# Optimization experiments

Hardware: AMD Instinct MI355X
Metric: run time of the kernel (lower is better)

## Reference

```python
import jax, jax.numpy as jnp
import numpy as np

B, H, W, C, HID, V, EMB = 16, 24, 96, 1024, 256, 5000, 256
BN_EPS = 1e-5


def _lin(k, fin, fout, s=0.05):
    return jax.random.normal(k, (fin, fout), jnp.float32) * s


def setup_inputs():
    ks = jax.random.split(jax.random.key(0), 24)
    inp = {
        "input_y": jax.random.randint(ks[0], (B,), 0, V),
        "input_hidden": jax.random.normal(ks[1], (B, 1, HID), jnp.float32),
        "img_feature": jax.random.normal(ks[2], (B, C, H, W), jnp.float32),
        "feature_w": W,
        "attention_sum": jnp.zeros((B, 1, H, W), jnp.float32),
        "alpha_t": jax.random.uniform(ks[3], (B, 1, H, W), jnp.float32),
        "feature_h": H,
        "batch_size": B,
        "h_mask": jax.random.randint(ks[4], (B,), 1, H + 1),
        "w_mask": jax.random.randint(ks[5], (B,), 1, W + 1),
        "emb_table": jax.random.normal(ks[6], (V, EMB), jnp.float32) * 0.05,
        "gru1_wi": _lin(ks[7], EMB, 3 * HID), "gru1_wh": _lin(ks[8], HID, 3 * HID),
        "gru1_bi": jnp.zeros((3 * HID,), jnp.float32), "gru1_bh": jnp.zeros((3 * HID,), jnp.float32),
        "fc1_w": _lin(ks[9], HID, 256), "fc1_b": jnp.zeros((256,), jnp.float32),
        "gru2_wi": _lin(ks[10], C, 3 * HID), "gru2_wh": _lin(ks[11], HID, 3 * HID),
        "gru2_bi": jnp.zeros((3 * HID,), jnp.float32), "gru2_bh": jnp.zeros((3 * HID,), jnp.float32),
        "out_w": _lin(ks[12], 128, V), "out_b": jnp.zeros((V,), jnp.float32),
        "emb2_w": _lin(ks[13], 256, 128), "emb2_b": jnp.zeros((128,), jnp.float32),
        "conv1_w": jax.random.normal(ks[14], (1, 1, 3, 3), jnp.float32) * 0.05,
        "conv1_b": jnp.zeros((1,), jnp.float32),
        "conv_tan_w": jax.random.normal(ks[15], (256, 256, 3, 3), jnp.float32) * 0.02,
        "conv_tan_b": jnp.zeros((256,), jnp.float32),
        "fc2_w": _lin(ks[16], HID, 128), "fc2_b": jnp.zeros((128,), jnp.float32),
        "ua_w": _lin(ks[17], C, 256), "ua_b": jnp.zeros((256,), jnp.float32),
        "uf_w": _lin(ks[18], 1, 256), "uf_b": jnp.zeros((256,), jnp.float32),
        "v_w": _lin(ks[19], 256, 1), "v_b": jnp.zeros((1,), jnp.float32),
        "wc_w": _lin(ks[20], C, 128), "wc_b": jnp.zeros((128,), jnp.float32),
        "bn1_gamma": jnp.ones((256,), jnp.float32), "bn1_beta": jnp.zeros((256,), jnp.float32),
        "bn1_mean": jnp.zeros((256,), jnp.float32), "bn1_var": jnp.ones((256,), jnp.float32),
    }
    return inp


def _gru(x, h, wi, wh, bi, bh):
    # PyTorch GRUCell semantics
    gi = x @ wi + bi
    gh = h @ wh + bh
    ir, iz, inn = jnp.split(gi, 3, axis=-1)
    hr, hz, hn = jnp.split(gh, 3, axis=-1)
    r = jax.nn.sigmoid(ir + hr)
    z = jax.nn.sigmoid(iz + hz)
    n = jnp.tanh(inn + r * hn)
    return (1.0 - z) * n + z * h


def _conv(x, w, b):
    y = jax.lax.conv_general_dilated(x, w, (1, 1), 'SAME',
                                     dimension_numbers=('NCHW', 'OIHW', 'NCHW'))
    return y + b[None, :, None, None]


def reference(input_y, input_hidden, img_feature, feature_w, attention_sum, alpha_t,
              feature_h, batch_size, h_mask, w_mask,
              emb_table, gru1_wi, gru1_wh, gru1_bi, gru1_bh, fc1_w, fc1_b,
              gru2_wi, gru2_wh, gru2_bi, gru2_bh, out_w, out_b, emb2_w, emb2_b,
              conv1_w, conv1_b, conv_tan_w, conv_tan_b, fc2_w, fc2_b,
              ua_w, ua_b, uf_w, uf_b, v_w, v_b, wc_w, wc_b,
              bn1_gamma, bn1_beta, bn1_mean, bn1_var):
    b, c, h, w = img_feature.shape
    # per-sample validity mask over the feature map  [B, H, W]
    et_mask = ((jnp.arange(h)[None, :] < h_mask[:, None])[:, :, None]
               & (jnp.arange(w)[None, :] < w_mask[:, None])[:, None, :]).astype(jnp.float32)

    emb = emb_table[input_y]                      # [B, 256] (dropout = identity, eval)
    h0 = input_hidden[:, 0, :]                    # [B, HID]
    st1 = _gru(emb, h0, gru1_wi, gru1_wh, gru1_bi, gru1_bh)
    st1 = st1 @ fc1_w + fc1_b                     # [B, 256]

    alpha_c = _conv(alpha_t, conv1_w, conv1_b)    # [B, 1, H, W]
    att_sum = attention_sum + alpha_c             # coverage accumulator

    img1 = jnp.einsum('bchw,cd->bhwd', img_feature, ua_w) + ua_b  # [B,H,W,256]
    att1 = att_sum[:, 0, :, :, None] * uf_w[0] + uf_b             # Linear(1,256)
    et = st1[:, None, None, :] + img1 + att1      # [B, H, W, 256]

    et_nchw = jnp.transpose(et, (0, 3, 1, 2))
    et_nchw = _conv(et_nchw, conv_tan_w, conv_tan_b)
    et_nchw = et_nchw * et_mask[:, None]
    inv = bn1_gamma / jnp.sqrt(bn1_var + BN_EPS)  # eval-mode BatchNorm2d(256)
    et_nchw = (et_nchw - bn1_mean[None, :, None, None]) * inv[None, :, None, None] \
              + bn1_beta[None, :, None, None]
    et_nchw = jnp.tanh(et_nchw)

    e = jnp.einsum('bchw,c->bhw', et_nchw, v_w[:, 0]) + v_b[0]    # [B, H, W]
    e_exp = jnp.exp(e) * et_mask
    e_sum = jnp.sum(e_exp, axis=(1, 2))
    alpha = e_exp / (e_sum[:, None, None] + 1e-8)                 # masked softmax

    ct = jnp.einsum('bhw,bchw->bc', alpha, img_feature)           # [B, 1024]
    st = _gru(ct, st1, gru2_wi, gru2_wh, gru2_bi, gru2_bh)        # [B, HID]
    hidden_next = st[:, None, :]

    pre = (st @ fc2_w + fc2_b) + (emb @ emb2_w + emb2_b) + (ct @ wc_w + wc_b)  # [B,128]
    output = jax.nn.log_softmax(pre @ out_w + out_b, axis=1)[:, None, :]       # [B,1,V]
    return output, hidden_next, alpha[:, None], att_sum
```

## Files before the change

kernel.cpp:

```cpp
#include <hip/hip_runtime.h>
#include <hip/hip_bf16.h>

#define B   16
#define H   24
#define W   96
#define C   1024
#define HID 256
#define V   5000
#define EMB 256
#define HW  (H*W)
#define BN_EPS 1e-5f
#define H2  (H+2)
#define W2  (W+2)

#define OUT0 0
#define OUT1 (B*V)
#define OUT2 (OUT1 + B*HID)
#define OUT3 (OUT2 + B*HW)

#define WSB_IMGT  0
#define WSB_ETP   75497472
#define WSB_WTB   96370688
#define WSB_UAT   97550336
#define WSB_E     98074624
#define WSB_ST1   98369536
#define WSB_CT    98385920
#define WSB_PRE   98451456
#define WSB_GIGH1 98459648
#define WSB_GH2   98574336
#define WSB_GI2   98631680

typedef __attribute__((ext_vector_type(8))) short short8;
typedef __attribute__((ext_vector_type(4))) float f32x4;

__device__ inline unsigned short f2bf(float f) {
    union { float f; unsigned int u; } v; v.f = f;
    unsigned int r = v.u + 0x7fffu + ((v.u >> 16) & 1u);
    return (unsigned short)(r >> 16);
}
__device__ inline float bf2f(unsigned short u) {
    union { unsigned int u; float f; } v; v.u = ((unsigned int)u) << 16;
    return v.f;
}

__global__ __launch_bounds__(256) void k_imgT(const float* img, unsigned short* imgT)
{
    int hw0 = blockIdx.x*64, c0 = blockIdx.y*128, b = blockIdx.z;
    int t = threadIdx.x;
    __shared__ __align__(16) unsigned short tr[64*256];
    int row = t & 63;
    int sgb = t >> 6;
    const float* src = img + ((size_t)b*C + c0)*HW + hw0 + row;
    #pragma unroll
    for (int k = 0; k < 4; ++k) {
        int sg = sgb + k*4;
        union { short8 v; unsigned short u[8]; } pk;
        #pragma unroll
        for (int j = 0; j < 8; ++j)
            pk.u[j] = f2bf(src[(size_t)(sg*8 + j)*HW]);
        *(short8*)&tr[row*256 + (sg ^ (row & 31))*8] = pk.v;
    }
    __syncthreads();
    #pragma unroll
    for (int k = 0; k < 4; ++k) {
        int i = k*256 + t;
        int orow = i >> 4, sg = i & 15;
        *(short8*)&imgT[((size_t)(b*HW) + hw0 + orow)*1024 + c0 + sg*8] =
            *(const short8*)&tr[orow*256 + (sg ^ (orow & 31))*8];
    }
}

__global__ __launch_bounds__(256) void k_prep(
    const float* conv_w_src, unsigned short* wtb,
    const float* ua_w, unsigned short* uat,
    const float* att_in, const float* alpha_t, const float* cw, const float* cb, float* att_out,
    float* ct, unsigned short* et_p)
{
    int x = blockIdx.x, t = threadIdx.x;
    if (x < 2304) {
        int idx = x*256 + t;
        int c = idx & 255; int o = (idx >> 8) & 255; int khw = idx >> 16;
        wtb[(khw*256 + o)*256 + c] = f2bf(conv_w_src[(o*256 + c)*9 + khw]);
    } else if (x < 3328) {
        int idx = (x - 2304)*256 + t;
        int c = idx & 1023; int d = idx >> 10;
        uat[d*1024 + c] = f2bf(ua_w[c*256 + d]);
    } else if (x < 3472) {
        int i = (x - 3328)*256 + t;
        int w = i % W; int h = (i / W) % H; int b = i / HW;
        float s = cb[0];
        #pragma unroll
        for (int kh = 0; kh < 3; ++kh) {
            int r = h + kh - 1; if (r < 0 || r >= H) continue;
            #pragma unroll
            for (int kw = 0; kw < 3; ++kw) {
                int c = w + kw - 1; if (c < 0 || c >= W) continue;
                s += alpha_t[(b*H + r)*W + c]*cw[kh*3+kw];
            }
        }
        att_out[i] = att_in[i] + s;
    } else if (x < 3536) {
        ct[(x - 3472)*256 + t] = 0.f;
    } else {
        int flat = (x - 3536)*256 + t;
        int b = flat / 7808; int r = flat - b*7808;
        int h2, w2, j;
        if (r < 3136)      { h2 = 0;  w2 = r >> 5;          j = r & 31; }
        else if (r < 6272) { h2 = 25; w2 = (r - 3136) >> 5; j = (r - 3136) & 31; }
        else {
            int rr = r - 6272;
            h2 = 1 + (rr >> 6);
            int s = rr & 63;
            w2 = (s < 32) ? 0 : 97;
            j = s & 31;
        }
        ((int4*)et_p)[((size_t)(b*H2 + h2)*W2 + w2)*32 + j] = make_int4(0,0,0,0);
    }
}

__global__ __launch_bounds__(256) void k_tail1(
    const int* y, const float* emb_table, const float* h0,
    const float* wi, const float* wh, float* gigh)
{
    int virt = blockIdx.x*16;
    int t = threadIdx.x;
    bool gi_mode = virt < 768;
    __shared__ float a_l[16*256];
    for (int i = t; i < 4096; i += 256) {
        int b = i >> 8, k = i & 255;
        a_l[i] = gi_mode ? emb_table[y[b]*EMB + k] : h0[b*HID + k];
    }
    __syncthreads();
    int nl = t & 15, b = t >> 4;
    int n = (gi_mode ? virt : virt - 768) + nl;
    const float* wp = gi_mode ? wi : wh;
    float acc = 0.f;
    #pragma unroll 16
    for (int k = 0; k < 256; ++k) acc += a_l[b*256 + k]*wp[k*768 + n];
    gigh[b*1536 + virt + nl] = acc;
}

__global__ __launch_bounds__(256) void k_fc1c(
    const float* gigh, const float* h0, const float* bi, const float* bh,
    const float* fc1_w, const float* fc1_b, float* st1)
{
    int n0 = blockIdx.x*16, t = threadIdx.x;
    __shared__ float a_l[16*256];
    for (int i = t; i < 4096; i += 256) {
        int b = i >> 8, k = i & 255;
        const float* g = gigh + b*1536;
        float ir = g[k] + bi[k], iz = g[256+k] + bi[256+k], in_ = g[512+k] + bi[512+k];
        float hr = g[768+k] + bh[k], hz = g[1024+k] + bh[256+k], hn = g[1280+k] + bh[512+k];
        float r = 1.f/(1.f+__expf(-(ir+hr)));
        float z = 1.f/(1.f+__expf(-(iz+hz)));
        float n = tanhf(in_ + r*hn);
        a_l[i] = (1.f - z)*n + z*h0[b*HID + k];
    }
    __syncthreads();
    int nl = t & 15, b = t >> 4;
    float acc = fc1_b[n0+nl];
    #pragma unroll 16
    for (int k = 0; k < 256; ++k) acc += a_l[b*256+k]*fc1_w[k*256 + n0 + nl];
    st1[b*256 + n0 + nl] = acc;
}

__global__ __launch_bounds__(256, 3) void k_et(
    const unsigned short* imgT, const unsigned short* uat, const float* ua_b,
    const float* st1, const float* att_sum, const float* uf_w, const float* uf_b,
    unsigned short* et_p)
{
    int h = blockIdx.x, ny = blockIdx.y, b = blockIdx.z;
    int t = threadIdx.x;
    int wv = t >> 6, lane = t & 63, q = lane >> 4, ln = lane & 15;
    int n0 = ny*128 + wv*32;
    __shared__ __align__(16) unsigned short a_l[96*256];

    f32x4 acc[12];
    #pragma unroll
    for (int i = 0; i < 12; ++i) acc[i] = (f32x4){0.f,0.f,0.f,0.f};

    const unsigned short* ab = imgT + ((size_t)(b*HW) + h*W)*1024;
    const unsigned short* bbase = uat + (size_t)(n0 + ln)*1024 + q*8;

    int sw8 = (q ^ ((ln & 7) << 2)) << 3;
    int ebase[6];
    #pragma unroll
    for (int mf = 0; mf < 6; ++mf) ebase[mf] = (ln + 16*mf)*256 + sw8;

    for (int c0 = 0; c0 < 1024; c0 += 128) {
        __syncthreads();
        #pragma unroll
        for (int i = t; i < 1536; i += 256) {
            int m = i >> 4, sg = i & 15;
            ((int4*)a_l)[m*32 + (sg ^ ((m & 7) << 2))] =
                *((const int4*)(ab + (size_t)m*1024 + c0) + sg);
        }
        __syncthreads();
        #pragma unroll
        for (int cs = 0; cs < 128; cs += 32) {
            short8 av[6];
            #pragma unroll
            for (int mf = 0; mf < 6; ++mf)
                av[mf] = *(const short8*)&a_l[ebase[mf] ^ cs];
            #pragma unroll
            for (int j = 0; j < 2; ++j) {
                short8 bv = *(const short8*)(bbase + (size_t)(j*16)*1024 + c0 + cs);
                #pragma unroll
                for (int mf = 0; mf < 6; ++mf)
                    acc[mf*2+j] = __builtin_amdgcn_mfma_f32_16x16x32_bf16(av[mf], bv, acc[mf*2+j], 0, 0, 0);
            }
        }
    }

    float att_m[24];
    #pragma unroll
    for (int mf = 0; mf < 6; ++mf)
        #pragma unroll
        for (int r = 0; r < 4; ++r)
            att_m[mf*4+r] = att_sum[(b*H + h)*W + mf*16 + q*4 + r];
    #pragma unroll
    for (int j = 0; j < 2; ++j) {
        int n = n0 + j*16 + ln;
        float s1 = st1[b*256 + n] + ua_b[n];
        float ufw = uf_w[n], ufb = uf_b[n];
        #pragma unroll
        for (int mf = 0; mf < 6; ++mf)
            #pragma unroll
            for (int r = 0; r < 4; ++r) {
                int m = mf*16 + q*4 + r;
                float v = acc[mf*2+j][r] + s1 + att_m[mf*4+r]*ufw + ufb;
                et_p[((size_t)(b*H2 + h + 1)*W2 + (m + 1))*256 + n] = f2bf(v);
            }
    }
}

__global__ __launch_bounds__(256, 3) void k_conv(
    const unsigned short* et_p, const unsigned short* wtb, const float* cb,
    const float* bn_g, const float* bn_b, const float* bn_m, const float* bn_v,
    const float* v_w, float* e_part)
{
    int h = blockIdx.x, ny = blockIdx.y, b = blockIdx.z;
    int t = threadIdx.x;
    int wv = t >> 6, lane = t & 63, q = lane >> 4, ln = lane & 15;
    int n0 = ny*128 + wv*32;
    __shared__ __align__(16) unsigned short patch[3*6400];
    __shared__ float lds_red[4][96];

    f32x4 acc[12];
    #pragma unroll
    for (int i = 0; i < 12; ++i) acc[i] = (f32x4){0.f,0.f,0.f,0.f};

    int abase[6][3];
    #pragma unroll
    for (int mf = 0; mf < 6; ++mf)
        #pragma unroll
        for (int kw = 0; kw < 3; ++kw) {
            int x2 = ln + 16*mf + kw;
            int sp0 = ((x2 & 3) << 3) | (q ^ (((x2 >> 2) & 3) << 1));
            abase[mf][kw] = (x2 >> 2)*256 + sp0*8;
        }

    for (int c0 = 0; c0 < 256; c0 += 64) {
        __syncthreads();
        for (int i = t; i < 2352; i += 256) {
            int kh = i / 784; int r = i - kh*784; int x2 = r >> 3; int sg = r & 7;
            const int4* src = (const int4*)et_p + ((size_t)(b*H2 + h + kh)*W2 + x2)*32 + (c0 >> 3) + sg;
            int sp = ((x2 & 3) << 3) | (sg ^ (((x2 >> 2) & 3) << 1));
            ((int4*)patch)[kh*800 + (x2 >> 2)*32 + sp] = *src;
        }
        __syncthreads();
        #pragma unroll
        for (int kh = 0; kh < 3; ++kh) {
            #pragma unroll
            for (int kw = 0; kw < 3; ++kw) {
                const unsigned short* brow = wtb + ((size_t)((kh*3 + kw)*256 + n0 + ln))*256 + c0 + q*8;
                #pragma unroll
                for (int cs = 0; cs < 64; cs += 32) {
                    short8 av[6];
                    #pragma unroll
                    for (int mf = 0; mf < 6; ++mf)
                        av[mf] = *(const short8*)&patch[kh*6400 + (abase[mf][kw] ^ cs)];
                    #pragma unroll
                    for (int j = 0; j < 2; ++j) {
                        short8 bv = *(const short8*)(brow + j*4096 + cs);
                        #pragma unroll
                        for (int mf = 0; mf < 6; ++mf)
                            acc[mf*2+j] = __builtin_amdgcn_mfma_f32_16x16x32_bf16(av[mf], bv, acc[mf*2+j], 0, 0, 0);
                    }
                }
            }
        }
    }

    float psum[24];
    #pragma unroll
    for (int i = 0; i < 24; ++i) psum[i] = 0.f;
    #pragma unroll
    for (int j = 0; j < 2; ++j) {
        int o = n0 + j*16 + ln;
        float inv  = bn_g[o]*rsqrtf(bn_v[o] + BN_EPS);
        float mean = bn_m[o], beta = bn_b[o], bias = cb[o], vw = v_w[o];
        #pragma unroll
        for (int mf = 0; mf < 6; ++mf)
            #pragma unroll
            for (int r = 0; r < 4; ++r) {
                float x = (acc[mf*2+j][r] + bias - mean)*inv + beta;
                x = fminf(fmaxf(x, -15.f), 15.f);
                float ex = __expf(2.f*x);
                psum[mf*4+r] += ((ex - 1.f)/(ex + 1.f))*vw;
            }
    }
    #pragma unroll
    for (int s = 1; s < 16; s <<= 1)
        #pragma unroll
        for (int i = 0; i < 24; ++i) psum[i] += __shfl_xor(psum[i], s);
    if (ln == 0) {
        #pragma unroll
        for (int mf = 0; mf < 6; ++mf)
            #pragma unroll
            for (int r = 0; r < 4; ++r)
                lds_red[wv][mf*16 + q*4 + r] = psum[mf*4+r];
    }
    __syncthreads();
    if (t < 96)
        e_part[(size_t)ny*(B*HW) + (b*H + h)*W + t] =
            lds_red[0][t] + lds_red[1][t] + lds_red[2][t] + lds_red[3][t];
}

__global__ __launch_bounds__(256) void k_softmax(
    const float* e_part, const int* h_mask, const int* w_mask, const float* v_b,
    float* alpha_out)
{
    int b = blockIdx.x, t = threadIdx.x;
    int hm = h_mask[b], wm = w_mask[b];
    float vb = v_b[0];
    __shared__ float red[256];
    float vals[9];
    float loc = 0.f;
    #pragma unroll
    for (int i = 0; i < 9; ++i) {
        int hw = t + i*256;
        int hh = hw / W, ww = hw % W;
        float v = 0.f;
        if (hh < hm && ww < wm)
            v = __expf(e_part[b*HW + hw] + e_part[B*HW + b*HW + hw] + vb);
        vals[i] = v; loc += v;
    }
    red[t] = loc; __syncthreads();
    for (int s = 128; s > 0; s >>= 1) { if (t < s) red[t] += red[t+s]; __syncthreads(); }
    float inv = 1.f/(red[0] + 1e-8f);
    #pragma unroll
    for (int i = 0; i < 9; ++i) alpha_out[b*HW + t + i*256] = vals[i]*inv;
}

__global__ __launch_bounds__(256) void k_ct(
    const float* alpha, const unsigned short* imgT, float* ct)
{
    int s = blockIdx.x, b = blockIdx.y, t = threadIdx.x;
    int cg = (t & 127)*8, half = t >> 7;
    float acc[8];
    #pragma unroll
    for (int j = 0; j < 8; ++j) acc[j] = 0.f;
    for (int i = 0; i < 72; ++i) {
        int hw = s*144 + i*2 + half;
        float a = alpha[b*HW + hw];
        union { short8 v; unsigned short u[8]; } pk;
        pk.v = *(const short8*)&imgT[((size_t)(b*HW) + hw)*1024 + cg];
        #pragma unroll
        for (int j = 0; j < 8; ++j) acc[j] += a*bf2f(pk.u[j]);
    }
    #pragma unroll
    for (int j = 0; j < 8; ++j) atomicAdd(&ct[b*1024 + cg + j], acc[j]);
}

__global__ __launch_bounds__(256) void k_g2(
    const float* st1, const int* y, const float* emb_table,
    const float* wh, const float* emb2_w, float* gh2,
    const float* ct, const float* wi, const float* wc_w, float* gi2p)
{
    int x = blockIdx.x, t = threadIdx.x;
    __shared__ float a_l[16*256];
    if (x < 56) {
        int virt = x*16;
        bool ghm = virt < 768;
        for (int i = t; i < 4096; i += 256) {
            int b = i >> 8, k = i & 255;
            a_l[i] = ghm ? st1[b*256 + k] : emb_table[y[b]*EMB + k];
        }
        __syncthreads();
        int nl = t & 15, b = t >> 4;
        float acc = 0.f;
        if (ghm) {
            int n = virt + nl;
            #pragma unroll 16
            for (int k = 0; k < 256; ++k) acc += a_l[b*256+k]*wh[k*768 + n];
        } else {
            int n = virt - 768 + nl;
            #pragma unroll 16
            for (int k = 0; k < 256; ++k) acc += a_l[b*256+k]*emb2_w[k*128 + n];
        }
        gh2[b*896 + virt + nl] = acc;
    } else {
        int xx = x - 56;
        int ks = xx / 56, virt = (xx - ks*56)*16;
        int k0 = ks*256;
        for (int i = t; i < 4096; i += 256) {
            int b = i >> 8, k = i & 255;
            a_l[i] = ct[b*1024 + k0 + k];
        }
        __syncthreads();
        int nl = t & 15, b = t >> 4;
        float acc = 0.f;
        if (virt < 768) {
            int n = virt + nl;
            #pragma unroll 16
            for (int k = 0; k < 256; ++k) acc += a_l[b*256+k]*wi[(k0+k)*768 + n];
        } else {
            int n = virt - 768 + nl;
            #pragma unroll 16
            for (int k = 0; k < 256; ++k) acc += a_l[b*256+k]*wc_w[(k0+k)*128 + n];
        }
        gi2p[(ks*16 + b)*896 + virt + nl] = acc;
    }
}

__global__ __launch_bounds__(256) void k_fc2c(
    const float* gi2p, const float* gh2, const float* st1,
    const float* bi, const float* bh,
    const float* fc2_w, const float* fc2_b, const float* emb2_b, const float* wc_b,
    float* hidden_out, float* pre)
{
    int n0 = blockIdx.x*16, t = threadIdx.x;
    __shared__ float st_l[16*256];
    for (int i = t; i < 4096; i += 256) {
        int b = i >> 8, k = i & 255;
        float ir = bi[k], iz = bi[256+k], in_ = bi[512+k];
        #pragma unroll
        for (int ks = 0; ks < 4; ++ks) {
            const float* g = gi2p + (ks*16 + b)*896;
            ir += g[k]; iz += g[256+k]; in_ += g[512+k];
        }
        const float* gh = gh2 + b*896;
        float hr = gh[k] + bh[k], hz = gh[256+k] + bh[256+k], hn = gh[512+k] + bh[512+k];
        float h = st1[b*256+k];
        float r = 1.f/(1.f+__expf(-(ir+hr)));
        float z = 1.f/(1.f+__expf(-(iz+hz)));
        float n = tanhf(in_ + r*hn);
        float s = (1.f - z)*n + z*h;
        st_l[i] = s;
        if (blockIdx.x == 0) hidden_out[b*HID + k] = s;
    }
    __syncthreads();
    int nl = t & 15, b = t >> 4;
    int n = n0 + nl;
    float acc = fc2_b[n] + emb2_b[n] + wc_b[n] + gh2[b*896 + 768 + n];
    #pragma unroll
    for (int ks = 0; ks < 4; ++ks) acc += gi2p[(ks*16 + b)*896 + 768 + n];
    #pragma unroll 16
    for (int k = 0; k < 256; ++k) acc += st_l[b*256+k]*fc2_w[k*128 + n];
    pre[b*128 + n] = acc;
}

__global__ __launch_bounds__(256) void k_logits(
    const float* pre, const float* out_w, const float* out_b, float* out)
{
    int j0 = blockIdx.x*64, t = threadIdx.x;
    __shared__ float pre_l[16*128];
    for (int i = t; i < 2048; i += 256) pre_l[i] = pre[i];
    __syncthreads();
    int jl = t & 63, bg = t >> 6;
    int j = j0 + jl;
    if (j >= V) return;
    float acc0=0.f, acc1=0.f, acc2=0.f, acc3=0.f;
    const float* pl = pre_l + bg*4*128;
    #pragma unroll 8
    for (int k = 0; k < 128; ++k) {
        float wv = out_w[k*V + j];
        acc0 += pl[k]*wv; acc1 += pl[128+k]*wv; acc2 += pl[256+k]*wv; acc3 += pl[384+k]*wv;
    }
    float ob = out_b[j];
    out[(bg*4+0)*V + j] = acc0 + ob;
    out[(bg*4+1)*V + j] = acc1 + ob;
    out[(bg*4+2)*V + j] = acc2 + ob;
    out[(bg*4+3)*V + j] = acc3 + ob;
}

__global__ __launch_bounds__(1024) void k_lsm(float* out)
{
    int b = blockIdx.x, t = threadIdx.x;
    __shared__ float red[1024];
    float lg[5]; float mx = -1e30f;
    #pragma unroll
    for (int i = 0; i < 5; ++i) {
        int j = t + i*1024;
        lg[i] = (j < V) ? out[b*V + j] : -1e30f;
        mx = fmaxf(mx, lg[i]);
    }
    red[t] = mx; __syncthreads();
    for (int s = 512; s > 0; s >>= 1) { if (t < s) red[t] = fmaxf(red[t], red[t+s]); __syncthreads(); }
    float gmax = red[0]; __syncthreads();
    float se = 0.f;
    #pragma unroll
    for (int i = 0; i < 5; ++i) { int j = t + i*1024; if (j < V) se += __expf(lg[i] - gmax); }
    red[t] = se; __syncthreads();
    for (int s = 512; s > 0; s >>= 1) { if (t < s) red[t] += red[t+s]; __syncthreads(); }
    float lse = logf(red[0]);
    #pragma unroll
    for (int i = 0; i < 5; ++i) { int j = t + i*1024; if (j < V) out[b*V + j] = lg[i] - gmax - lse; }
}

extern "C" void kernel_launch(void* const* d_in, const int* in_sizes, int n_in,
                              void* d_out, int out_size, void* d_ws, size_t ws_size,
                              hipStream_t stream)
{
    const int*   input_y      = (const int*)  d_in[0];
    const float* input_hidden = (const float*)d_in[1];
    const float* img          = (const float*)d_in[2];
    const float* attention    = (const float*)d_in[4];
    const float* alpha_t      = (const float*)d_in[5];
    const int*   h_mask       = (const int*)  d_in[8];
    const int*   w_mask       = (const int*)  d_in[9];
    const float* emb_table    = (const float*)d_in[10];
    const float* gru1_wi      = (const float*)d_in[11];
    const float* gru1_wh      = (const float*)d_in[12];
    const float* gru1_bi      = (const float*)d_in[13];
    const float* gru1_bh      = (const float*)d_in[14];
    const float* fc1_w        = (const float*)d_in[15];
    const float* fc1_b        = (const float*)d_in[16];
    const float* gru2_wi      = (const float*)d_in[17];
    const float* gru2_wh      = (const float*)d_in[18];
    const float* gru2_bi      = (const float*)d_in[19];
    const float* gru2_bh      = (const float*)d_in[20];
    const float* out_w        = (const float*)d_in[21];
    const float* out_b        = (const float*)d_in[22];
    const float* emb2_w       = (const float*)d_in[23];
    const float* emb2_b       = (const float*)d_in[24];
    const float* conv1_w      = (const float*)d_in[25];
    const float* conv1_b      = (const float*)d_in[26];
    const float* conv_tan_w   = (const float*)d_in[27];
    const float* conv_tan_b   = (const float*)d_in[28];
    const float* fc2_w        = (const float*)d_in[29];
    const float* fc2_b        = (const float*)d_in[30];
    const float* ua_w         = (const float*)d_in[31];
    const float* ua_b         = (const float*)d_in[32];
    const float* uf_w         = (const float*)d_in[33];
    const float* uf_b         = (const float*)d_in[34];
    const float* v_w          = (const float*)d_in[35];
    const float* v_b          = (const float*)d_in[36];
    const float* wc_w         = (const float*)d_in[37];
    const float* wc_b         = (const float*)d_in[38];
    const float* bn1_gamma    = (const float*)d_in[39];
    const float* bn1_beta     = (const float*)d_in[40];
    const float* bn1_mean     = (const float*)d_in[41];
    const float* bn1_var      = (const float*)d_in[42];

    float* out = (float*)d_out;
    char*  ws  = (char*)d_ws;
    unsigned short* imgT = (unsigned short*)(ws + WSB_IMGT);
    unsigned short* et_p = (unsigned short*)(ws + WSB_ETP);
    unsigned short* wtb  = (unsigned short*)(ws + WSB_WTB);
    unsigned short* uat  = (unsigned short*)(ws + WSB_UAT);
    float* e_part = (float*)(ws + WSB_E);
    float* st1   = (float*)(ws + WSB_ST1);
    float* ct    = (float*)(ws + WSB_CT);
    float* pre   = (float*)(ws + WSB_PRE);
    float* gigh1 = (float*)(ws + WSB_GIGH1);
    float* gh2   = (float*)(ws + WSB_GH2);
    float* gi2p  = (float*)(ws + WSB_GI2);

    float* out_logits = out + OUT0;
    float* out_hidden = out + OUT1;
    float* out_alpha  = out + OUT2;
    float* out_attsum = out + OUT3;

    k_imgT<<<dim3(HW/64, C/128, B), 256, 0, stream>>>(img, imgT);
    k_prep<<<4024, 256, 0, stream>>>(conv_tan_w, wtb, ua_w, uat,
                                     attention, alpha_t, conv1_w, conv1_b, out_attsum,
                                     ct, et_p);
    k_tail1<<<96, 256, 0, stream>>>(input_y, emb_table, input_hidden,
                                    gru1_wi, gru1_wh, gigh1);
    k_fc1c<<<16, 256, 0, stream>>>(gigh1, input_hidden, gru1_bi, gru1_bh,
                                   fc1_w, fc1_b, st1);
    k_et<<<dim3(H, 2, B), 256, 0, stream>>>(imgT, uat, ua_b, st1, out_attsum,
                                            uf_w, uf_b, et_p);
    k_conv<<<dim3(H, 2, B), 256, 0, stream>>>(et_p, wtb, conv_tan_b,
                                              bn1_gamma, bn1_beta, bn1_mean, bn1_var,
                                              v_w, e_part);
    k_softmax<<<B, 256, 0, stream>>>(e_part, h_mask, w_mask, v_b, out_alpha);
    k_ct<<<dim3(16, B), 256, 0, stream>>>(out_alpha, imgT, ct);
    k_g2<<<280, 256, 0, stream>>>(st1, input_y, emb_table, gru2_wh, emb2_w, gh2,
                                  ct, gru2_wi, wc_w, gi2p);
    k_fc2c<<<8, 256, 0, stream>>>(gi2p, gh2, st1, gru2_bi, gru2_bh,
                                  fc2_w, fc2_b, emb2_b, wc_b, out_hidden, pre);
    k_logits<<<(V + 63)/64, 256, 0, stream>>>(pre, out_w, out_b, out_logits);
    k_lsm<<<B, 1024, 0, stream>>>(out_logits);
}
```

Before: 546.9 us.

## Retile et/conv GEMMs to 2x2 wave grid and register-prefetch next LDS tile

Both the et projection and conv kernels change their per-wave tiling from 96 rows x 32 columns to a 2x2 wave grid of 48 rows x 64 columns each. This loads fewer A fragments from LDS per MFMA and reuses each global B fragment across fewer rows. The next K-chunk of the A tile is now prefetched into registers while the MFMAs of the current chunk run, so global load latency overlaps compute. The LDS swizzle patterns are also changed. The cost is higher register pressure from the prefetch buffers (10 int4 in conv), which may lower occupancy under launch_bounds(256,3).

```diff
diff --git a/kernel.cpp b/kernel.cpp
--- a/kernel.cpp
+++ b/kernel.cpp
@@ -172,7 +172,8 @@
     int h = blockIdx.x, ny = blockIdx.y, b = blockIdx.z;
     int t = threadIdx.x;
     int wv = t >> 6, lane = t & 63, q = lane >> 4, ln = lane & 15;
-    int n0 = ny*128 + wv*32;
+    int wm = wv & 1, wn = wv >> 1;
+    int n0 = ny*128 + wn*64;
     __shared__ __align__(16) unsigned short a_l[96*256];
 
     f32x4 acc[12];
@@ -182,53 +183,70 @@
     const unsigned short* ab = imgT + ((size_t)(b*HW) + h*W)*1024;
     const unsigned short* bbase = uat + (size_t)(n0 + ln)*1024 + q*8;
 
-    int sw8 = (q ^ ((ln & 7) << 2)) << 3;
-    int ebase[6];
-    #pragma unroll
-    for (int mf = 0; mf < 6; ++mf) ebase[mf] = (ln + 16*mf)*256 + sw8;
+    int slot0 = q ^ (ln & 7);
+    int ebase[3];
+    #pragma unroll
+    for (int mf = 0; mf < 3; ++mf)
+        ebase[mf] = (wm*48 + ln + 16*mf)*256 + slot0*8;
+
+    int4 pr[6];
+    #pragma unroll
+    for (int k = 0; k < 6; ++k) {
+        int i = t + k*256;
+        int m = i >> 4, sg = i & 15;
+        pr[k] = *((const int4*)(ab + (size_t)m*1024) + sg);
+    }
 
     for (int c0 = 0; c0 < 1024; c0 += 128) {
         __syncthreads();
         #pragma unroll
-        for (int i = t; i < 1536; i += 256) {
+        for (int k = 0; k < 6; ++k) {
+            int i = t + k*256;
             int m = i >> 4, sg = i & 15;
-            ((int4*)a_l)[m*32 + (sg ^ ((m & 7) << 2))] =
-                *((const int4*)(ab + (size_t)m*1024 + c0) + sg);
+            ((int4*)a_l)[m*32 + ((sg & 8) | ((sg ^ m) & 7))] = pr[k];
         }
         __syncthreads();
+        if (c0 < 896) {
+            #pragma unroll
+            for (int k = 0; k < 6; ++k) {
+                int i = t + k*256;
+                int m = i >> 4, sg = i & 15;
+                pr[k] = *((const int4*)(ab + (size_t)m*1024 + c0 + 128) + sg);
+            }
+        }
         #pragma unroll
         for (int cs = 0; cs < 128; cs += 32) {
-            short8 av[6];
-            #pragma unroll
-            for (int mf = 0; mf < 6; ++mf)
+            short8 av[3];
+            #pragma unroll
+            for (int mf = 0; mf < 3; ++mf)
                 av[mf] = *(const short8*)&a_l[ebase[mf] ^ cs];
             #pragma unroll
-            for (int j = 0; j < 2; ++j) {
+            for (int j = 0; j < 4; ++j) {
                 short8 bv = *(const short8*)(bbase + (size_t)(j*16)*1024 + c0 + cs);
                 #pragma unroll
-                for (int mf = 0; mf < 6; ++mf)
-                    acc[mf*2+j] = __builtin_amdgcn_mfma_f32_16x16x32_bf16(av[mf], bv, acc[mf*2+j], 0, 0, 0);
-            }
-        }
-    }
-
-    float att_m[24];
-    #pragma unroll
-    for (int mf = 0; mf < 6; ++mf)
+                for (int mf = 0; mf < 3; ++mf)
+                    acc[mf*4+j] = __builtin_amdgcn_mfma_f32_16x16x32_bf16(av[mf], bv, acc[mf*4+j], 0, 0, 0);
+            }
+        }
+    }
+
+    float att_m[12];
+    #pragma unroll
+    for (int mf = 0; mf < 3; ++mf)
         #pragma unroll
         for (int r = 0; r < 4; ++r)
-            att_m[mf*4+r] = att_sum[(b*H + h)*W + mf*16 + q*4 + r];
-    #pragma unroll
-    for (int j = 0; j < 2; ++j) {
+            att_m[mf*4+r] = att_sum[(b*H + h)*W + wm*48 + mf*16 + q*4 + r];
+    #pragma unroll
+    for (int j = 0; j < 4; ++j) {
         int n = n0 + j*16 + ln;
         float s1 = st1[b*256 + n] + ua_b[n];
         float ufw = uf_w[n], ufb = uf_b[n];
         #pragma unroll
-        for (int mf = 0; mf < 6; ++mf)
+        for (int mf = 0; mf < 3; ++mf)
             #pragma unroll
             for (int r = 0; r < 4; ++r) {
-                int m = mf*16 + q*4 + r;
-                float v = acc[mf*2+j][r] + s1 + att_m[mf*4+r]*ufw + ufb;
+                int m = wm*48 + mf*16 + q*4 + r;
+                float v = acc[mf*4+j][r] + s1 + att_m[mf*4+r]*ufw + ufb;
                 et_p[((size_t)(b*H2 + h + 1)*W2 + (m + 1))*256 + n] = f2bf(v);
             }
     }
@@ -242,33 +260,59 @@
     int h = blockIdx.x, ny = blockIdx.y, b = blockIdx.z;
     int t = threadIdx.x;
     int wv = t >> 6, lane = t & 63, q = lane >> 4, ln = lane & 15;
-    int n0 = ny*128 + wv*32;
+    int wm = wv & 1, wn = wv >> 1;
+    int n0 = ny*128 + wn*64;
     __shared__ __align__(16) unsigned short patch[3*6400];
-    __shared__ float lds_red[4][96];
+    __shared__ float lds_red[2][96];
 
     f32x4 acc[12];
     #pragma unroll
     for (int i = 0; i < 12; ++i) acc[i] = (f32x4){0.f,0.f,0.f,0.f};
 
-    int abase[6][3];
-    #pragma unroll
-    for (int mf = 0; mf < 6; ++mf)
+    int abase[3][3];
+    #pragma unroll
+    for (int mf = 0; mf < 3; ++mf)
         #pragma unroll
         for (int kw = 0; kw < 3; ++kw) {
-            int x2 = ln + 16*mf + kw;
-            int sp0 = ((x2 & 3) << 3) | (q ^ (((x2 >> 2) & 3) << 1));
+            int x2 = wm*48 + ln + 16*mf + kw;
+            int sp0 = ((x2 & 3) << 3) | ((q ^ (x2 & 7)) & 7);
             abase[mf][kw] = (x2 >> 2)*256 + sp0*8;
         }
+
+    const int4* ebase_g = (const int4*)et_p;
+
+    int4 pr[10];
+    #pragma unroll
+    for (int k = 0; k < 10; ++k) {
+        int i = t + k*256;
+        if (i < 2352) {
+            int kh = i / 784; int r = i - kh*784; int x2 = r >> 3; int sg = r & 7;
+            pr[k] = ebase_g[((size_t)(b*H2 + h + kh)*W2 + x2)*32 + sg];
+        }
+    }
 
     for (int c0 = 0; c0 < 256; c0 += 64) {
         __syncthreads();
-        for (int i = t; i < 2352; i += 256) {
-            int kh = i / 784; int r = i - kh*784; int x2 = r >> 3; int sg = r & 7;
-            const int4* src = (const int4*)et_p + ((size_t)(b*H2 + h + kh)*W2 + x2)*32 + (c0 >> 3) + sg;
-            int sp = ((x2 & 3) << 3) | (sg ^ (((x2 >> 2) & 3) << 1));
-            ((int4*)patch)[kh*800 + (x2 >> 2)*32 + sp] = *src;
+        #pragma unroll
+        for (int k = 0; k < 10; ++k) {
+            int i = t + k*256;
+            if (i < 2352) {
+                int kh = i / 784; int r = i - kh*784; int x2 = r >> 3; int sg = r & 7;
+                int sp = ((x2 & 3) << 3) | ((sg ^ (x2 & 7)) & 7);
+                ((int4*)patch)[kh*800 + (x2 >> 2)*32 + sp] = pr[k];
+            }
         }
         __syncthreads();
+        if (c0 < 192) {
+            #pragma unroll
+            for (int k = 0; k < 10; ++k) {
+                int i = t + k*256;
+                if (i < 2352) {
+                    int kh = i / 784; int r = i - kh*784; int x2 = r >> 3; int sg = r & 7;
+                    pr[k] = ebase_g[((size_t)(b*H2 + h + kh)*W2 + x2)*32 + ((c0 + 64) >> 3) + sg];
+                }
+            }
+        }
         #pragma unroll
         for (int kh = 0; kh < 3; ++kh) {
             #pragma unroll
@@ -276,35 +320,35 @@
                 const unsigned short* brow = wtb + ((size_t)((kh*3 + kw)*256 + n0 + ln))*256 + c0 + q*8;
                 #pragma unroll
                 for (int cs = 0; cs < 64; cs += 32) {
-                    short8 av[6];
+                    short8 av[3];
                     #pragma unroll
-                    for (int mf = 0; mf < 6; ++mf)
+                    for (int mf = 0; mf < 3; ++mf)
                         av[mf] = *(const short8*)&patch[kh*6400 + (abase[mf][kw] ^ cs)];
                     #pragma unroll
-                    for (int j = 0; j < 2; ++j) {
+                    for (int j = 0; j < 4; ++j) {
                         short8 bv = *(const short8*)(brow + j*4096 + cs);
                         #pragma unroll
-                        for (int mf = 0; mf < 6; ++mf)
-                            acc[mf*2+j] = __builtin_amdgcn_mfma_f32_16x16x32_bf16(av[mf], bv, acc[mf*2+j], 0, 0, 0);
+                        for (int mf = 0; mf < 3; ++mf)
+                            acc[mf*4+j] = __builtin_amdgcn_mfma_f32_16x16x32_bf16(av[mf], bv, acc[mf*4+j], 0, 0, 0);
                     }
                 }
             }
         }
     }
 
-    float psum[24];
-    #pragma unroll
-    for (int i = 0; i < 24; ++i) psum[i] = 0.f;
-    #pragma unroll
-    for (int j = 0; j < 2; ++j) {
+    float psum[12];
+    #pragma unroll
+    for (int i = 0; i < 12; ++i) psum[i] = 0.f;
+    #pragma unroll
+    for (int j = 0; j < 4; ++j) {
         int o = n0 + j*16 + ln;
         float inv  = bn_g[o]*rsqrtf(bn_v[o] + BN_EPS);
         float mean = bn_m[o], beta = bn_b[o], bias = cb[o], vw = v_w[o];
         #pragma unroll
-        for (int mf = 0; mf < 6; ++mf)
+        for (int mf = 0; mf < 3; ++mf)
             #pragma unroll
             for (int r = 0; r < 4; ++r) {
-                float x = (acc[mf*2+j][r] + bias - mean)*inv + beta;
+                float x = (acc[mf*4+j][r] + bias - mean)*inv + beta;
                 x = fminf(fmaxf(x, -15.f), 15.f);
                 float ex = __expf(2.f*x);
                 psum[mf*4+r] += ((ex - 1.f)/(ex + 1.f))*vw;
@@ -313,18 +357,17 @@
     #pragma unroll
     for (int s = 1; s < 16; s <<= 1)
         #pragma unroll
-        for (int i = 0; i < 24; ++i) psum[i] += __shfl_xor(psum[i], s);
+        for (int i = 0; i < 12; ++i) psum[i] += __shfl_xor(psum[i], s);
     if (ln == 0) {
         #pragma unroll
-        for (int mf = 0; mf < 6; ++mf)
+        for (int mf = 0; mf < 3; ++mf)
             #pragma unroll
             for (int r = 0; r < 4; ++r)
-                lds_red[wv][mf*16 + q*4 + r] = psum[mf*4+r];
+                lds_red[wn][wm*48 + mf*16 + q*4 + r] = psum[mf*4+r];
     }
     __syncthreads();
     if (t < 96)
-        e_part[(size_t)ny*(B*HW) + (b*H + h)*W + t] =
-            lds_red[0][t] + lds_red[1][t] + lds_red[2][t] + lds_red[3][t];
+        e_part[(size_t)ny*(B*HW) + (b*H + h)*W + t] = lds_red[0][t] + lds_red[1][t];
 }
 
 __global__ __launch_bounds__(256) void k_softmax(
```

Result: slower. 660.0 us (+20.7%).

## Repack bf16 weights into k-chunk-major layout and swizzle global reads into compact LDS

Applied to the files above, without the earlier changes.

The conv and ua weight matrices are now stored in a layout of 8-element channel chunks by output index, so the B-operand loads of the 16 lanes in a quad fall on adjacent 16-byte blocks and coalesce. The LDS staging in k_et and k_conv drops its padded layout. It applies the XOR swizzle on the global-read side and stores densely, which shrinks LDS use in k_et and should allow higher occupancy. The risk is less coalesced global reads for the A operand, because the XORed chunk order scatters each row's accesses.

```diff
diff --git a/kernel.cpp b/kernel.cpp
--- a/kernel.cpp
+++ b/kernel.cpp
@@ -80,11 +80,12 @@
     if (x < 2304) {
         int idx = x*256 + t;
         int c = idx & 255; int o = (idx >> 8) & 255; int khw = idx >> 16;
-        wtb[(khw*256 + o)*256 + c] = f2bf(conv_w_src[(o*256 + c)*9 + khw]);
+        wtb[(((size_t)khw*32 + (c >> 3))*256 + o)*8 + (c & 7)] =
+            f2bf(conv_w_src[(o*256 + c)*9 + khw]);
     } else if (x < 3328) {
         int idx = (x - 2304)*256 + t;
         int c = idx & 1023; int d = idx >> 10;
-        uat[d*1024 + c] = f2bf(ua_w[c*256 + d]);
+        uat[((size_t)(c >> 3)*256 + d)*8 + (c & 7)] = f2bf(ua_w[c*256 + d]);
     } else if (x < 3472) {
         int i = (x - 3328)*256 + t;
         int w = i % W; int h = (i / W) % H; int b = i / HW;
@@ -173,27 +174,29 @@
     int t = threadIdx.x;
     int wv = t >> 6, lane = t & 63, q = lane >> 4, ln = lane & 15;
     int n0 = ny*128 + wv*32;
-    __shared__ __align__(16) unsigned short a_l[96*256];
+    __shared__ __align__(16) unsigned short a_l[96*128];
 
     f32x4 acc[12];
     #pragma unroll
     for (int i = 0; i < 12; ++i) acc[i] = (f32x4){0.f,0.f,0.f,0.f};
 
     const unsigned short* ab = imgT + ((size_t)(b*HW) + h*W)*1024;
-    const unsigned short* bbase = uat + (size_t)(n0 + ln)*1024 + q*8;
-
-    int sw8 = (q ^ ((ln & 7) << 2)) << 3;
+
     int ebase[6];
     #pragma unroll
-    for (int mf = 0; mf < 6; ++mf) ebase[mf] = (ln + 16*mf)*256 + sw8;
+    for (int mf = 0; mf < 6; ++mf) {
+        int m = ln + 16*mf;
+        ebase[mf] = m*128 + (q ^ (m & 7))*8;
+    }
 
     for (int c0 = 0; c0 < 1024; c0 += 128) {
         __syncthreads();
         #pragma unroll
-        for (int i = t; i < 1536; i += 256) {
-            int m = i >> 4, sg = i & 15;
-            ((int4*)a_l)[m*32 + (sg ^ ((m & 7) << 2))] =
-                *((const int4*)(ab + (size_t)m*1024 + c0) + sg);
+        for (int k = 0; k < 6; ++k) {
+            int i = t + k*256;
+            int m = i >> 4, s = i & 15;
+            ((int4*)a_l)[m*16 + s] =
+                *((const int4*)(ab + (size_t)m*1024 + c0) + (s ^ (m & 7)));
         }
         __syncthreads();
         #pragma unroll
@@ -202,9 +205,11 @@
             #pragma unroll
             for (int mf = 0; mf < 6; ++mf)
                 av[mf] = *(const short8*)&a_l[ebase[mf] ^ cs];
+            const unsigned short* bp =
+                uat + ((size_t)(((c0 + cs) >> 3) + q)*256 + n0 + ln)*8;
             #pragma unroll
             for (int j = 0; j < 2; ++j) {
-                short8 bv = *(const short8*)(bbase + (size_t)(j*16)*1024 + c0 + cs);
+                short8 bv = *(const short8*)(bp + j*128);
                 #pragma unroll
                 for (int mf = 0; mf < 6; ++mf)
                     acc[mf*2+j] = __builtin_amdgcn_mfma_f32_16x16x32_bf16(av[mf], bv, acc[mf*2+j], 0, 0, 0);
@@ -243,7 +248,7 @@
     int t = threadIdx.x;
     int wv = t >> 6, lane = t & 63, q = lane >> 4, ln = lane & 15;
     int n0 = ny*128 + wv*32;
-    __shared__ __align__(16) unsigned short patch[3*6400];
+    __shared__ __align__(16) unsigned short patch[3*98*64];
     __shared__ float lds_red[4][96];
 
     f32x4 acc[12];
@@ -256,33 +261,35 @@
         #pragma unroll
         for (int kw = 0; kw < 3; ++kw) {
             int x2 = ln + 16*mf + kw;
-            int sp0 = ((x2 & 3) << 3) | (q ^ (((x2 >> 2) & 3) << 1));
-            abase[mf][kw] = (x2 >> 2)*256 + sp0*8;
-        }
+            abase[mf][kw] = x2*64 + (q ^ (x2 & 7))*8;
+        }
+
+    const int4* gsrc = (const int4*)et_p;
 
     for (int c0 = 0; c0 < 256; c0 += 64) {
         __syncthreads();
         for (int i = t; i < 2352; i += 256) {
-            int kh = i / 784; int r = i - kh*784; int x2 = r >> 3; int sg = r & 7;
-            const int4* src = (const int4*)et_p + ((size_t)(b*H2 + h + kh)*W2 + x2)*32 + (c0 >> 3) + sg;
-            int sp = ((x2 & 3) << 3) | (sg ^ (((x2 >> 2) & 3) << 1));
-            ((int4*)patch)[kh*800 + (x2 >> 2)*32 + sp] = *src;
+            int kh = i / 784; int r = i - kh*784; int x2 = r >> 3; int s = r & 7;
+            ((int4*)patch)[kh*784 + x2*8 + s] =
+                gsrc[((size_t)(b*H2 + h + kh)*W2 + x2)*32 + (c0 >> 3) + (s ^ (x2 & 7))];
         }
         __syncthreads();
         #pragma unroll
         for (int kh = 0; kh < 3; ++kh) {
             #pragma unroll
             for (int kw = 0; kw < 3; ++kw) {
-                const unsigned short* brow = wtb + ((size_t)((kh*3 + kw)*256 + n0 + ln))*256 + c0 + q*8;
                 #pragma unroll
                 for (int cs = 0; cs < 64; cs += 32) {
                     short8 av[6];
                     #pragma unroll
                     for (int mf = 0; mf < 6; ++mf)
-                        av[mf] = *(const short8*)&patch[kh*6400 + (abase[mf][kw] ^ cs)];
+                        av[mf] = *(const short8*)&patch[kh*6272 + (abase[mf][kw] ^ cs)];
+                    const unsigned short* bp = wtb
+                        + (size_t)(kh*3 + kw)*65536
+                        + ((size_t)(((c0 + cs) >> 3) + q)*256 + n0 + ln)*8;
                     #pragma unroll
                     for (int j = 0; j < 2; ++j) {
-                        short8 bv = *(const short8*)(brow + j*4096 + cs);
+                        short8 bv = *(const short8*)(bp + j*128);
                         #pragma unroll
                         for (int mf = 0; mf < 6; ++mf)
                             acc[mf*2+j] = __builtin_amdgcn_mfma_f32_16x16x32_bf16(av[mf], bv, acc[mf*2+j], 0, 0, 0);
```

Measured after the change: 534.2 us. -2.3%, faster.
